# Optimization experiments

Measured on AMD Instinct MI355X. Metric: run time of the kernel, lower is better.

## Reference

```python
import jax, jax.numpy as jnp
import numpy as np

L, B, N, D, H, INTER = 4, 64, 128, 1024, 16, 4096
HD = D // H
EPS = 1e-12


def layer_norm(x, g, b):
    m = jnp.mean(x, axis=-1, keepdims=True)
    v = jnp.mean(jnp.square(x - m), axis=-1, keepdims=True)
    return (x - m) * jax.lax.rsqrt(v + EPS) * g + b


def fast_self_attention(x, wq_w, wq_b, wk_w, wk_b, hwq, hwk, tr_w, tr_b):
    # x: [B, T, D]
    Bq, T, _ = x.shape
    q = x @ wq_w + wq_b                                  # [B,T,D]
    hq = q.reshape(Bq, T, H, HD).transpose(0, 2, 1, 3)    # [B,H,T,hd]
    # additive attention over queries (mask scores are all-zero here)
    alpha = jax.nn.softmax(jnp.einsum('bhtd,hd->bht', hq, hwq) / np.sqrt(HD), axis=-1)
    gq = jnp.einsum('bht,bhtd->bhd', alpha, hq).reshape(Bq, 1, D)  # global query [B,1,D]
    k = x @ wk_w + wk_b
    p = k * gq                                            # [B,T,D]
    hp = p.reshape(Bq, T, H, HD).transpose(0, 2, 1, 3)
    beta = jax.nn.softmax(jnp.einsum('bhtd,hd->bht', hp, hwk) / np.sqrt(HD), axis=-1)
    gk = jnp.einsum('bht,bhtd->bhd', beta, hp).reshape(Bq, 1, D)   # global key [B,1,D]
    u = q * gk
    r = u @ tr_w + tr_b
    return r + q


def encoder_layer(x, p, i):
    a = fast_self_attention(x, p['wq_w'][i], p['wq_b'][i], p['wk_w'][i], p['wk_b'][i],
                            p['hwq'][i], p['hwk'][i], p['tr_w'][i], p['tr_b'][i])
    a = a @ p['so_w'][i] + p['so_b'][i]
    a = layer_norm(a, p['ln1_g'][i], p['ln1_b'][i])
    h = jax.nn.gelu(a @ p['int_w'][i] + p['int_b'][i], approximate=False)
    o = h @ p['out_w'][i] + p['out_b'][i]
    return layer_norm(o + a, p['ln2_g'][i], p['ln2_b'][i])


def setup_inputs() -> dict:
    key = jax.random.key(0)
    ks = iter(jax.random.split(key, 32))
    s = 0.02
    inp = {
        'x': jax.random.normal(next(ks), (B, N, D), jnp.float32),
        'wq_w': jax.random.normal(next(ks), (L, D, D)) * s,
        'wq_b': jnp.zeros((L, D)),
        'wk_w': jax.random.normal(next(ks), (L, D, D)) * s,
        'wk_b': jnp.zeros((L, D)),
        'hwq': jax.random.normal(next(ks), (L, H, HD)) * s,
        'hwk': jax.random.normal(next(ks), (L, H, HD)) * s,
        'tr_w': jax.random.normal(next(ks), (L, D, D)) * s,
        'tr_b': jnp.zeros((L, D)),
        'so_w': jax.random.normal(next(ks), (L, D, D)) * s,
        'so_b': jnp.zeros((L, D)),
        'ln1_g': jnp.ones((L, D)),
        'ln1_b': jnp.zeros((L, D)),
        'int_w': jax.random.normal(next(ks), (L, D, INTER)) * s,
        'int_b': jnp.zeros((L, INTER)),
        'out_w': jax.random.normal(next(ks), (L, INTER, D)) * s,
        'out_b': jnp.zeros((L, D)),
        'ln2_g': jnp.ones((L, D)),
        'ln2_b': jnp.zeros((L, D)),
        'pool_w': jax.random.normal(next(ks), (D, D)) * s,
        'pool_b': jnp.zeros((D,)),
        'pool_q': jax.random.normal(next(ks), (D,)) * s,
    }
    return inp


def reference(x, wq_w, wq_b, wk_w, wk_b, hwq, hwk, tr_w, tr_b, so_w, so_b,
              ln1_g, ln1_b, int_w, int_b, out_w, out_b, ln2_g, ln2_b,
              pool_w, pool_b, pool_q):
    p = dict(wq_w=wq_w, wq_b=wq_b, wk_w=wk_w, wk_b=wk_b, hwq=hwq, hwk=hwk,
             tr_w=tr_w, tr_b=tr_b, so_w=so_w, so_b=so_b, ln1_g=ln1_g, ln1_b=ln1_b,
             int_w=int_w, int_b=int_b, out_w=out_w, out_b=out_b, ln2_g=ln2_g, ln2_b=ln2_b)
    h = x
    for i in range(L):
        h = encoder_layer(h, p, i)
    # additive attention pooling (mask scores are zeros)
    scores = jnp.tanh(h @ pool_w + pool_b) @ pool_q       # [B,N]
    w = jax.nn.softmax(scores, axis=-1)
    return jnp.einsum('bn,bnd->bd', w, h)                 # [B,D]
```

## Files before the change

### kernel.cpp

```cpp
#include <hip/hip_runtime.h>
#include <hip/hip_bf16.h>
#include <math.h>

typedef unsigned short u16;
typedef __attribute__((ext_vector_type(4))) unsigned short u16x4;
typedef __attribute__((ext_vector_type(8))) unsigned short u16x8;
typedef __attribute__((ext_vector_type(8))) short s16x8;
typedef __attribute__((ext_vector_type(4))) float f32x4;

typedef const __attribute__((address_space(1))) void* gas_t;
typedef __attribute__((address_space(3))) void* las_t;

#define DI __device__ __forceinline__

static constexpr int Bc = 64, Nc = 128, Dc = 1024, Hc = 16, HDc = 64, Ic = 4096, Lc = 4;
static constexpr int Mrows = Bc * Nc;

DI float b2f(u16 u) { union { unsigned i; float f; } x; x.i = ((unsigned)u) << 16; return x.f; }
DI u16 f2b(float f) {
  union { float f; unsigned i; } x; x.f = f;
  unsigned r = x.i + 0x7FFF + ((x.i >> 16) & 1);
  return (u16)(r >> 16);
}

#define BARRIER do { asm volatile("" ::: "memory"); __builtin_amdgcn_s_barrier(); asm volatile("" ::: "memory"); } while (0)
#define VMC(N) asm volatile("s_waitcnt vmcnt(" #N ")" ::: "memory")

#define STG(PTR, ROW0, T, SLOT) do { \
    const u16* _s = (PTR) + (size_t)((ROW0) + srow) * K + (((T) << 6) + scol); \
    __builtin_amdgcn_global_load_lds((gas_t)_s, (las_t)(smem + (SLOT) + ldsw), 16, 0, 0); \
    __builtin_amdgcn_global_load_lds((gas_t)(_s + ((size_t)K << 3)), (las_t)(smem + (SLOT) + ldsw + 1024), 16, 0, 0); \
  } while (0)

#define LDA(BUFB, RH) do { \
    _Pragma("unroll") \
    for (int mi = 0; mi < 4; ++mi) { \
      af[mi][0] = *(const s16x8*)(smem + (BUFB) + Abase_rd + (RH) * 8192 + mi * 2048 + aoff0); \
      af[mi][1] = *(const s16x8*)(smem + (BUFB) + Abase_rd + (RH) * 8192 + mi * 2048 + aoff1); \
    } } while (0)

#define LDB(DST, BUFB, CH) do { \
    _Pragma("unroll") \
    for (int nj = 0; nj < 2; ++nj) { \
      DST[nj][0] = *(const s16x8*)(smem + (BUFB) + Bbase_rd + (CH) * 4096 + nj * 2048 + aoff0); \
      DST[nj][1] = *(const s16x8*)(smem + (BUFB) + Bbase_rd + (CH) * 4096 + nj * 2048 + aoff1); \
    } } while (0)

#define MFMAQ(RH, CH, BF) do { \
    __builtin_amdgcn_s_setprio(1); \
    _Pragma("unroll") \
    for (int kk = 0; kk < 2; ++kk) \
      _Pragma("unroll") \
      for (int mi = 0; mi < 4; ++mi) \
        _Pragma("unroll") \
        for (int nj = 0; nj < 2; ++nj) \
          acc[(RH) * 4 + mi][(CH) * 2 + nj] = __builtin_amdgcn_mfma_f32_16x16x32_bf16( \
              af[mi][kk], BF[nj][kk], acc[(RH) * 4 + mi][(CH) * 2 + nj], 0, 0, 0); \
    __builtin_amdgcn_s_setprio(0); \
  } while (0)

template <int EPI, bool SPLIT>
__global__ __launch_bounds__(512, 2) void gemm256(
    const u16* __restrict__ A, const u16* __restrict__ BT,
    const float* __restrict__ bias, const float* __restrict__ bias2,
    const u16* __restrict__ resid, u16* __restrict__ C, u16* __restrict__ C2,
    int M, int N, int K, int NC) {
  extern __shared__ __align__(16) char smem[];
  const int tid = threadIdx.x;
  const int l = tid & 63;
  const int w = tid >> 6;
  const int wr = w >> 2, wc = w & 3;

  const int GX = gridDim.x;
  int wg = blockIdx.y * GX + blockIdx.x;
  const int nwg = GX * gridDim.y;
  wg = (wg & 7) * (nwg >> 3) + (wg >> 3);
  const int bn0 = (wg % GX) * 256;
  const int bm0 = (wg / GX) * 256;

  const int NT = K >> 6;
  const int NI = NT >> 1;

  const int row_l = l & 15;
  const int kl = (l >> 4) * 8;
  const int xr = (row_l & 7) << 3;
  const int aoff0 = row_l * 128 + (((0 * 32 + kl) ^ xr) * 2);
  const int aoff1 = row_l * 128 + (((1 * 32 + kl) ^ xr) * 2);
  const int Abase_rd = wr * 16384;
  const int Bbase_rd = 32768 + (wc >> 1) * 16384 + (wc & 1) * 8192;

  const int srow = w * 16 + (l >> 3);
  const int scol = ((l & 7) ^ ((l >> 3) & 7)) << 3;
  const int ldsw = w * 2048;

  enum { b0A0 = 0, b0A1 = 16384, b0B0 = 32768, b0B1 = 49152,
         b1A0 = 65536, b1A1 = 81920, b1B0 = 98304, b1B1 = 114688 };

  STG(BT, bn0, 0, b0B0);
  STG(BT, bn0 + 128, 0, b0B1);
  STG(A, bm0, 0, b0A0);
  STG(A, bm0 + 128, 0, b0A1);
  STG(BT, bn0, 1, b1B0);
  STG(BT, bn0 + 128, 1, b1B1);
  VMC(4);
  BARRIER;

  f32x4 acc[8][4];
#pragma unroll
  for (int i = 0; i < 8; ++i)
#pragma unroll
    for (int j = 0; j < 4; ++j) acc[i][j] = f32x4{0.f, 0.f, 0.f, 0.f};
  s16x8 af[4][2], bf0[2][2], bf1[2][2];

  for (int j = 0; j < NI; ++j) {
    const int t1 = 2 * j + 1;
    int t2 = 2 * j + 2; if (t2 >= NT) t2 = 0;
    int t3 = 2 * j + 3; if (t3 >= NT) t3 = 1;
    LDA(0, 0); LDB(bf0, 0, 0);
    STG(A, bm0, t1, b1A0);
    BARRIER; MFMAQ(0, 0, bf0); BARRIER;
    LDB(bf1, 0, 1);
    STG(A, bm0 + 128, t1, b1A1);
    BARRIER; MFMAQ(0, 1, bf1); BARRIER;
    LDA(0, 1);
    STG(BT, bn0, t2, b0B0);
    BARRIER; MFMAQ(1, 0, bf0); BARRIER;
    STG(BT, bn0 + 128, t2, b0B1);
    STG(A, bm0, t2, b0A0);
    VMC(6);
    BARRIER; MFMAQ(1, 1, bf1); BARRIER;
    LDA(65536, 0); LDB(bf0, 65536, 0);
    STG(A, bm0 + 128, t2, b0A1);
    BARRIER; MFMAQ(0, 0, bf0); BARRIER;
    LDB(bf1, 65536, 1);
    BARRIER; MFMAQ(0, 1, bf1); BARRIER;
    LDA(65536, 1);
    STG(BT, bn0, t3, b1B0);
    BARRIER; MFMAQ(1, 0, bf0); BARRIER;
    STG(BT, bn0 + 128, t3, b1B1);
    VMC(4);
    BARRIER; MFMAQ(1, 1, bf1); BARRIER;
  }

  u16* Cout = C;
  const float* bi = bias;
  int cb = bn0;
  if (SPLIT) {
    const int half = N >> 1;
    if (bn0 >= half) { Cout = C2; bi = bias2; cb = bn0 - half; }
  }
  const int r0 = bm0 + wr * 128 + ((l >> 4) << 2);
#pragma unroll
  for (int fi = 0; fi < 8; ++fi) {
#pragma unroll
    for (int fj = 0; fj < 4; ++fj) {
      const int ocol = cb + wc * 64 + fj * 16 + (l & 15);
      const float bv = bi[ocol];
      const int row = r0 + fi * 16;
#pragma unroll
      for (int r = 0; r < 4; ++r) {
        float v = acc[fi][fj][r] + bv;
        if constexpr (EPI == 1) v += b2f(resid[(size_t)(row + r) * NC + ocol]);
        if constexpr (EPI == 2) v = 0.5f * v * (1.f + erff(v * 0.70710678118654752f));
        if constexpr (EPI == 3) v = tanhf(v);
        Cout[(size_t)(row + r) * NC + ocol] = f2b(v);
      }
    }
  }
}

#define LDA2(BUFB, RH) do { \
    _Pragma("unroll") \
    for (int mi = 0; mi < 2; ++mi) { \
      af[mi][0] = *(const s16x8*)(smem + (BUFB) + Abase_rd + ((RH) * 2 + mi) * 2048 + aoff0); \
      af[mi][1] = *(const s16x8*)(smem + (BUFB) + Abase_rd + ((RH) * 2 + mi) * 2048 + aoff1); \
    } } while (0)

#define MFMAQ2(RH, CH, BF) do { \
    __builtin_amdgcn_s_setprio(1); \
    _Pragma("unroll") \
    for (int kk = 0; kk < 2; ++kk) \
      _Pragma("unroll") \
      for (int mi = 0; mi < 2; ++mi) \
        _Pragma("unroll") \
        for (int nj = 0; nj < 2; ++nj) \
          acc[(RH) * 2 + mi][(CH) * 2 + nj] = __builtin_amdgcn_mfma_f32_16x16x32_bf16( \
              af[mi][kk], BF[nj][kk], acc[(RH) * 2 + mi][(CH) * 2 + nj], 0, 0, 0); \
    __builtin_amdgcn_s_setprio(0); \
  } while (0)

template <int EPI>
__global__ __launch_bounds__(512, 2) void gemm128n(
    const u16* __restrict__ A, const u16* __restrict__ BT,
    const float* __restrict__ bias, const u16* __restrict__ resid,
    u16* __restrict__ C, int M, int N, int K, int NC) {
  extern __shared__ __align__(16) char smem[];
  const int tid = threadIdx.x;
  const int l = tid & 63;
  const int w = tid >> 6;
  const int wr = w >> 1, wc = w & 1;

  const int GX = gridDim.x;
  int wg = blockIdx.y * GX + blockIdx.x;
  const int nwg = GX * gridDim.y;
  wg = (wg & 7) * (nwg >> 3) + (wg >> 3);
  const int bn0 = (wg % GX) * 128;
  const int bm0 = (wg / GX) * 256;

  const int NT = K >> 6;
  const int NI = NT >> 1;

  const int row_l = l & 15;
  const int kl = (l >> 4) * 8;
  const int xr = (row_l & 7) << 3;
  const int aoff0 = row_l * 128 + (((0 * 32 + kl) ^ xr) * 2);
  const int aoff1 = row_l * 128 + (((1 * 32 + kl) ^ xr) * 2);
  const int Abase_rd = (wr >> 1) * 16384 + (wr & 1) * 8192;
  const int Bbase_rd = 32768 + wc * 8192;

  const int srow = w * 16 + (l >> 3);
  const int scol = ((l & 7) ^ ((l >> 3) & 7)) << 3;
  const int ldsw = w * 2048;

  enum { c0A0 = 0, c0A1 = 16384, c0B = 32768,
         c1A0 = 49152, c1A1 = 65536, c1B = 81920 };

  STG(BT, bn0, 0, c0B);
  STG(A, bm0, 0, c0A0);
  STG(A, bm0 + 128, 0, c0A1);
  STG(BT, bn0, 1, c1B);
  VMC(2);
  BARRIER;

  f32x4 acc[4][4];
#pragma unroll
  for (int i = 0; i < 4; ++i)
#pragma unroll
    for (int j = 0; j < 4; ++j) acc[i][j] = f32x4{0.f, 0.f, 0.f, 0.f};
  s16x8 af[2][2], bf0[2][2], bf1[2][2];

  for (int j = 0; j < NI; ++j) {
    const int t1 = 2 * j + 1;
    int t2 = 2 * j + 2; if (t2 >= NT) t2 = 0;
    int t3 = 2 * j + 3; if (t3 >= NT) t3 = 1;
    LDA2(0, 0); LDB(bf0, 0, 0);
    STG(A, bm0, t1, c1A0);
    BARRIER; MFMAQ2(0, 0, bf0); BARRIER;
    LDB(bf1, 0, 1);
    STG(A, bm0 + 128, t1, c1A1);
    BARRIER; MFMAQ2(0, 1, bf1); BARRIER;
    LDA2(0, 1);
    STG(BT, bn0, t2, c0B);
    BARRIER; MFMAQ2(1, 0, bf0); BARRIER;
    STG(A, bm0, t2, c0A0);
    VMC(4);
    BARRIER; MFMAQ2(1, 1, bf1); BARRIER;
    LDA2(49152, 0); LDB(bf0, 49152, 0);
    STG(A, bm0 + 128, t2, c0A1);
    BARRIER; MFMAQ2(0, 0, bf0); BARRIER;
    LDB(bf1, 49152, 1);
    BARRIER; MFMAQ2(0, 1, bf1); BARRIER;
    LDA2(49152, 1);
    STG(BT, bn0, t3, c1B);
    BARRIER; MFMAQ2(1, 0, bf0); BARRIER;
    VMC(2);
    BARRIER; MFMAQ2(1, 1, bf1); BARRIER;
  }

  const int r0 = bm0 + wr * 64 + ((l >> 4) << 2);
#pragma unroll
  for (int fi = 0; fi < 4; ++fi) {
#pragma unroll
    for (int fj = 0; fj < 4; ++fj) {
      const int ocol = bn0 + wc * 64 + fj * 16 + (l & 15);
      const float bv = bias[ocol];
      const int row = r0 + fi * 16;
#pragma unroll
      for (int r = 0; r < 4; ++r) {
        float v = acc[fi][fj][r] + bv;
        if constexpr (EPI == 1) v += b2f(resid[(size_t)(row + r) * NC + ocol]);
        if constexpr (EPI == 2) v = 0.5f * v * (1.f + erff(v * 0.70710678118654752f));
        if constexpr (EPI == 3) v = tanhf(v);
        C[(size_t)(row + r) * NC + ocol] = f2b(v);
      }
    }
  }
}

DI void ttile(const float* in, u16* out, int R, int C, int r0, int c0, int t) {
  __shared__ u16 tile[32][33];
  const int lr = t >> 3;
  const int lc = (t & 7) * 4;
  f32x4 v = *(const f32x4*)(in + (size_t)(r0 + lr) * C + c0 + lc);
#pragma unroll
  for (int j = 0; j < 4; ++j) tile[lr][lc + j] = f2b(v[j]);
  __syncthreads();
  u16x4 o;
#pragma unroll
  for (int j = 0; j < 4; ++j) o[j] = tile[lc + j][lr];
  *(u16x4*)(out + (size_t)(c0 + lr) * R + r0 + lc) = o;
}

__global__ __launch_bounds__(256) void transpose_cvt(
    const float* __restrict__ in, u16* __restrict__ out, int R, int C) {
  ttile(in, out, R, C, blockIdx.y * 32, blockIdx.x * 32, threadIdx.x);
}

__global__ __launch_bounds__(256) void transpose4sq(
    const float* s0, const float* s1, const float* s2, const float* s3,
    u16* d0, u16* d1, u16* d2, u16* d3) {
  const int z = blockIdx.z;
  const float* in = z == 0 ? s0 : z == 1 ? s1 : z == 2 ? s2 : s3;
  u16* out = z == 0 ? d0 : z == 1 ? d1 : z == 2 ? d2 : d3;
  ttile(in, out, 1024, 1024, blockIdx.y * 32, blockIdx.x * 32, threadIdx.x);
}

__global__ __launch_bounds__(256) void transpose_io(
    const float* si, u16* di, const float* so, u16* dout) {
  if (blockIdx.z == 0) {
    ttile(si, di, 1024, 4096, blockIdx.y * 32, blockIdx.x * 32, threadIdx.x);
  } else {
    ttile(so, dout, 4096, 1024, blockIdx.x * 32, blockIdx.y * 32, threadIdx.x);
  }
}

__global__ __launch_bounds__(256) void cvt_k(
    const float* __restrict__ in, u16* __restrict__ out) {
  const size_t i = ((size_t)blockIdx.x * 256 + threadIdx.x) * 8;
  f32x4 a = *(const f32x4*)(in + i);
  f32x4 b = *(const f32x4*)(in + i + 4);
  u16x8 o;
#pragma unroll
  for (int j = 0; j < 4; ++j) o[j] = f2b(a[j]);
#pragma unroll
  for (int j = 0; j < 4; ++j) o[4 + j] = f2b(b[j]);
  *(u16x8*)(out + i) = o;
}

__global__ __launch_bounds__(128) void attn_fused(
    const u16* __restrict__ q, const u16* __restrict__ k,
    const float* __restrict__ hwq, const float* __restrict__ hwk,
    u16* __restrict__ u) {
  const int bh = blockIdx.x;
  const int b = bh >> 4, h = bh & 15;
  const int tid = threadIdx.x;
  const int lane = tid & 63, wv = tid >> 6;
  const int d = tid & 63, half = tid >> 6;
  __shared__ u16 qt[128][68];
  __shared__ u16 kt[128][68];
  __shared__ float hw[64];
  __shared__ float gqs[64];
  __shared__ float gks[64];
  __shared__ float ex[128];
  __shared__ float part[64];
  __shared__ float xw[4];

  const int rw8 = tid >> 3;
  const int cg8 = (tid & 7) * 8;
#pragma unroll
  for (int pass = 0; pass < 8; ++pass) {
    const int row = pass * 16 + rw8;
    const size_t off = (size_t)(b * 128 + row) * Dc + h * 64 + cg8;
    u16x8 vq = *(const u16x8*)(q + off);
    u16x8 vk = *(const u16x8*)(k + off);
    u16x4 q0{vq[0], vq[1], vq[2], vq[3]}, q1{vq[4], vq[5], vq[6], vq[7]};
    u16x4 k0{vk[0], vk[1], vk[2], vk[3]}, k1{vk[4], vk[5], vk[6], vk[7]};
    *(u16x4*)&qt[row][cg8] = q0;
    *(u16x4*)&qt[row][cg8 + 4] = q1;
    *(u16x4*)&kt[row][cg8] = k0;
    *(u16x4*)&kt[row][cg8 + 4] = k1;
  }
  if (tid < 64) hw[tid] = hwq[h * 64 + tid];
  __syncthreads();

  float s = 0.f;
#pragma unroll
  for (int c = 0; c < 16; ++c) {
    u16x4 v = *(const u16x4*)&qt[tid][c * 4];
#pragma unroll
    for (int j = 0; j < 4; ++j) s += b2f(v[j]) * hw[c * 4 + j];
  }
  s *= 0.125f;
  float m = s;
  for (int o = 32; o; o >>= 1) m = fmaxf(m, __shfl_xor(m, o));
  if (lane == 0) xw[wv] = m;
  __syncthreads();
  m = fmaxf(xw[0], xw[1]);
  float e = __expf(s - m);
  ex[tid] = e;
  float sm = e;
  for (int o = 32; o; o >>= 1) sm += __shfl_xor(sm, o);
  if (lane == 0) xw[2 + wv] = sm;
  __syncthreads();
  float sum = xw[2] + xw[3];
  {
    float acc = 0.f;
    for (int t = 0; t < 64; ++t) acc += ex[half * 64 + t] * b2f(qt[half * 64 + t][d]);
    if (half == 0) part[d] = acc;
    __syncthreads();
    if (half == 1) gqs[d] = (part[d] + acc) / sum;
  }
  __syncthreads();

  if (tid < 64) hw[tid] = hwk[h * 64 + tid];
  __syncthreads();
  s = 0.f;
#pragma unroll
  for (int c = 0; c < 16; ++c) {
    u16x4 v = *(const u16x4*)&kt[tid][c * 4];
#pragma unroll
    for (int j = 0; j < 4; ++j) s += b2f(v[j]) * gqs[c * 4 + j] * hw[c * 4 + j];
  }
  s *= 0.125f;
  m = s;
  for (int o = 32; o; o >>= 1) m = fmaxf(m, __shfl_xor(m, o));
  if (lane == 0) xw[wv] = m;
  __syncthreads();
  m = fmaxf(xw[0], xw[1]);
  e = __expf(s - m);
  ex[tid] = e;
  sm = e;
  for (int o = 32; o; o >>= 1) sm += __shfl_xor(sm, o);
  if (lane == 0) xw[2 + wv] = sm;
  __syncthreads();
  sum = xw[2] + xw[3];
  {
    float acc = 0.f;
    for (int t = 0; t < 64; ++t) acc += ex[half * 64 + t] * b2f(kt[half * 64 + t][d]);
    acc *= gqs[d];
    if (half == 0) part[d] = acc;
    __syncthreads();
    if (half == 1) gks[d] = (part[d] + acc) / sum;
  }
  __syncthreads();

#pragma unroll
  for (int pass = 0; pass < 8; ++pass) {
    const int row = pass * 16 + rw8;
    u16x4 a = *(const u16x4*)&qt[row][cg8];
    u16x4 bb = *(const u16x4*)&qt[row][cg8 + 4];
    u16x8 o;
#pragma unroll
    for (int j = 0; j < 4; ++j) o[j] = f2b(b2f(a[j]) * gks[cg8 + j]);
#pragma unroll
    for (int j = 0; j < 4; ++j) o[4 + j] = f2b(b2f(bb[j]) * gks[cg8 + 4 + j]);
    *(u16x8*)(u + (size_t)(b * 128 + row) * Dc + h * 64 + cg8) = o;
  }
}

__global__ __launch_bounds__(256) void ln_k(
    const u16* __restrict__ in, const float* __restrict__ g,
    const float* __restrict__ bta, u16* __restrict__ out) {
  const int row = blockIdx.x, tid = threadIdx.x;
  const int lane = tid & 63, wave = tid >> 6;
  __shared__ float red[8];
  const u16* p = in + (size_t)row * Dc + tid * 4;
  u16x4 v = *(const u16x4*)p;
  float x[4];
  float s = 0.f, sq = 0.f;
#pragma unroll
  for (int j = 0; j < 4; ++j) {
    x[j] = b2f(v[j]);
    s += x[j];
    sq += x[j] * x[j];
  }
  for (int o = 32; o; o >>= 1) {
    s += __shfl_down(s, o);
    sq += __shfl_down(sq, o);
  }
  if (lane == 0) {
    red[wave] = s;
    red[4 + wave] = sq;
  }
  __syncthreads();
  s = red[0] + red[1] + red[2] + red[3];
  sq = red[4] + red[5] + red[6] + red[7];
  const float mean = s * (1.f / 1024.f);
  const float var = sq * (1.f / 1024.f) - mean * mean;
  const float rs = rsqrtf(var + 1e-12f);
  f32x4 gv = *(const f32x4*)(g + tid * 4);
  f32x4 bv = *(const f32x4*)(bta + tid * 4);
  u16x4 o;
#pragma unroll
  for (int j = 0; j < 4; ++j) o[j] = f2b((x[j] - mean) * rs * gv[j] + bv[j]);
  *(u16x4*)(out + (size_t)row * Dc + tid * 4) = o;
}

__global__ __launch_bounds__(256) void pool_k(
    const u16* __restrict__ s1, const float* __restrict__ pq,
    const u16* __restrict__ h, float* __restrict__ out) {
  const int b = blockIdx.x, tid = threadIdx.x;
  __shared__ float pqs[1024];
  __shared__ float sc[128];
  __shared__ float ex[128];
  for (int i = tid; i < 1024; i += 256) pqs[i] = pq[i];
  __syncthreads();
  if (tid < 128) {
    const u16* row = s1 + ((size_t)(b * 128 + tid)) * Dc;
    float s = 0.f;
    for (int c = 0; c < 128; ++c) {
      u16x8 v = *(const u16x8*)(row + c * 8);
#pragma unroll
      for (int j = 0; j < 8; ++j) s += b2f(v[j]) * pqs[c * 8 + j];
    }
    sc[tid] = s;
  }
  __syncthreads();
  float m = -1e30f;
  for (int t = 0; t < 128; ++t) m = fmaxf(m, sc[t]);
  if (tid < 128) ex[tid] = __expf(sc[tid] - m);
  __syncthreads();
  float sum = 0.f;
  for (int t = 0; t < 128; ++t) sum += ex[t];
  const int d0 = tid * 4;
  float acc[4] = {0.f, 0.f, 0.f, 0.f};
  for (int n = 0; n < 128; ++n) {
    const float w = ex[n];
    u16x4 v = *(const u16x4*)(h + ((size_t)(b * 128 + n)) * Dc + d0);
#pragma unroll
    for (int j = 0; j < 4; ++j) acc[j] += w * b2f(v[j]);
  }
  const float inv = 1.f / sum;
  f32x4 o;
#pragma unroll
  for (int j = 0; j < 4; ++j) o[j] = acc[j] * inv;
  *(f32x4*)(out + b * Dc + d0) = o;
}

extern "C" void kernel_launch(void* const* d_in, const int* in_sizes, int n_in,
                              void* d_out, int out_size, void* d_ws, size_t ws_size,
                              hipStream_t stream) {
  const float* x = (const float*)d_in[0];
  const float* wq_w = (const float*)d_in[1];
  const float* wq_b = (const float*)d_in[2];
  const float* wk_w = (const float*)d_in[3];
  const float* wk_b = (const float*)d_in[4];
  const float* hwq = (const float*)d_in[5];
  const float* hwk = (const float*)d_in[6];
  const float* tr_w = (const float*)d_in[7];
  const float* tr_b = (const float*)d_in[8];
  const float* so_w = (const float*)d_in[9];
  const float* so_b = (const float*)d_in[10];
  const float* ln1g = (const float*)d_in[11];
  const float* ln1b = (const float*)d_in[12];
  const float* int_w = (const float*)d_in[13];
  const float* int_b = (const float*)d_in[14];
  const float* out_w = (const float*)d_in[15];
  const float* out_b = (const float*)d_in[16];
  const float* ln2g = (const float*)d_in[17];
  const float* ln2b = (const float*)d_in[18];
  const float* pool_w = (const float*)d_in[19];
  const float* pool_b = (const float*)d_in[20];
  const float* pool_q = (const float*)d_in[21];

  char* w = (char*)d_ws;
  auto alloc = [&](size_t bytes) {
    char* p = w;
    w += (bytes + 255) & ~(size_t)255;
    return p;
  };
  u16* wTqk = (u16*)alloc((size_t)2 * Dc * Dc * 2);
  u16* wTtr = (u16*)alloc((size_t)Dc * Dc * 2);
  u16* wTso = (u16*)alloc((size_t)Dc * Dc * 2);
  u16* wTint = (u16*)alloc((size_t)Dc * Ic * 2);
  u16* wTout = (u16*)alloc((size_t)Dc * Ic * 2);
  u16* wTpool = (u16*)alloc((size_t)Dc * Dc * 2);
  u16* qb = (u16*)alloc((size_t)Mrows * Dc * 2);
  u16* kb = (u16*)alloc((size_t)Mrows * Dc * 2);
  u16* ab = (u16*)alloc((size_t)Mrows * Dc * 2);
  u16* tb = (u16*)alloc((size_t)Mrows * Dc * 2);
  u16* xc = (u16*)alloc((size_t)Mrows * Dc * 2);
  u16* hb = (u16*)alloc((size_t)Mrows * Ic * 2);
  if ((size_t)(w - (char*)d_ws) > ws_size) return;

  static constexpr size_t LDSB = 131072;
  static constexpr size_t LDSB2 = 98304;
  hipFuncSetAttribute((const void*)gemm256<0, true>, hipFuncAttributeMaxDynamicSharedMemorySize, LDSB);
  hipFuncSetAttribute((const void*)gemm256<2, false>, hipFuncAttributeMaxDynamicSharedMemorySize, LDSB);
  hipFuncSetAttribute((const void*)gemm128n<0>, hipFuncAttributeMaxDynamicSharedMemorySize, LDSB2);
  hipFuncSetAttribute((const void*)gemm128n<1>, hipFuncAttributeMaxDynamicSharedMemorySize, LDSB2);
  hipFuncSetAttribute((const void*)gemm128n<3>, hipFuncAttributeMaxDynamicSharedMemorySize, LDSB2);

  const dim3 blk(256);
  const dim3 blkG(512);
  const dim3 gT1(Dc / 32, Dc / 32);
  const dim3 gT4(Dc / 32, Dc / 32, 4);
  const dim3 gTio(Ic / 32, Dc / 32, 2);
  const dim3 gQK(2048 / 256, Mrows / 256);
  const dim3 gNi(Ic / 256, Mrows / 256);
  const dim3 gO(Dc / 128, Mrows / 256);

  cvt_k<<<(Mrows * Dc) / (256 * 8), blk, 0, stream>>>(x, xc);

  for (int i = 0; i < Lc; ++i) {
    transpose4sq<<<gT4, blk, 0, stream>>>(
        wq_w + (size_t)i * Dc * Dc, wk_w + (size_t)i * Dc * Dc,
        tr_w + (size_t)i * Dc * Dc, so_w + (size_t)i * Dc * Dc,
        wTqk, wTqk + (size_t)Dc * Dc, wTtr, wTso);
    transpose_io<<<gTio, blk, 0, stream>>>(
        int_w + (size_t)i * Dc * Ic, wTint, out_w + (size_t)i * Ic * Dc, wTout);

    gemm256<0, true><<<gQK, blkG, LDSB, stream>>>(xc, wTqk, wq_b + i * Dc, wk_b + i * Dc,
                                                  nullptr, qb, kb, Mrows, 2048, Dc, Dc);
    attn_fused<<<Bc * Hc, 128, 0, stream>>>(qb, kb, hwq + i * Hc * HDc,
                                            hwk + i * Hc * HDc, kb);
    gemm128n<1><<<gO, blkG, LDSB2, stream>>>(kb, wTtr, tr_b + i * Dc, qb, tb, Mrows, Dc, Dc, Dc);
    gemm128n<0><<<gO, blkG, LDSB2, stream>>>(tb, wTso, so_b + i * Dc, nullptr, kb, Mrows, Dc, Dc, Dc);
    ln_k<<<Mrows, blk, 0, stream>>>(kb, ln1g + i * Dc, ln1b + i * Dc, ab);
    gemm256<2, false><<<gNi, blkG, LDSB, stream>>>(ab, wTint, int_b + i * Ic, nullptr,
                                                   nullptr, hb, nullptr, Mrows, Ic, Dc, Ic);
    gemm128n<1><<<gO, blkG, LDSB2, stream>>>(hb, wTout, out_b + i * Dc, ab, tb, Mrows, Dc, Ic, Dc);
    ln_k<<<Mrows, blk, 0, stream>>>(tb, ln2g + i * Dc, ln2b + i * Dc, xc);
  }

  transpose_cvt<<<gT1, blk, 0, stream>>>(pool_w, wTpool, Dc, Dc);
  gemm128n<3><<<gO, blkG, LDSB2, stream>>>(xc, wTpool, pool_b, nullptr, tb, Mrows, Dc, Dc, Dc);
  pool_k<<<Bc, blk, 0, stream>>>(tb, pool_q, xc, (float*)d_out);
}
```

Before: 1.209 ms.

## Use 4-wave 256x256 GEMM with 128x128 per-wave tiles for QK and intermediate

Replaces the 8-wave (512-thread) 256x256 GEMM with a 4-wave (256-thread) variant in which each wave computes a 128x128 sub-tile (8x8 MFMA accumulators). Each thread now issues four direct-to-LDS loads per stage instead of two, and the vmcnt waits are adjusted to match. The goal is more MFMA work per LDS fragment load and fewer waves contending at barriers. The cost is far higher register pressure (256 accumulator floats per thread), one workgroup per CU, and less latency hiding.

After: 1.632 ms. 35.0% more time.

```diff
diff --git a/kernel.cpp b/kernel.cpp
--- a/kernel.cpp
+++ b/kernel.cpp
@@ -32,35 +32,43 @@
     __builtin_amdgcn_global_load_lds((gas_t)(_s + ((size_t)K << 3)), (las_t)(smem + (SLOT) + ldsw + 1024), 16, 0, 0); \
   } while (0)
 
-#define LDA(BUFB, RH) do { \
+#define STG4(PTR, ROW0, T, SLOT) do { \
+    const u16* _s = (PTR) + (size_t)((ROW0) + srow) * K + (((T) << 6) + scol); \
+    __builtin_amdgcn_global_load_lds((gas_t)_s, (las_t)(smem + (SLOT) + ldsw), 16, 0, 0); \
+    __builtin_amdgcn_global_load_lds((gas_t)(_s + ((size_t)K << 3)), (las_t)(smem + (SLOT) + ldsw + 1024), 16, 0, 0); \
+    __builtin_amdgcn_global_load_lds((gas_t)(_s + ((size_t)K << 4)), (las_t)(smem + (SLOT) + ldsw + 2048), 16, 0, 0); \
+    __builtin_amdgcn_global_load_lds((gas_t)(_s + 24 * (size_t)K), (las_t)(smem + (SLOT) + ldsw + 3072), 16, 0, 0); \
+  } while (0)
+
+#define LDAW(BUFB, RH) do { \
     _Pragma("unroll") \
     for (int mi = 0; mi < 4; ++mi) { \
       af[mi][0] = *(const s16x8*)(smem + (BUFB) + Abase_rd + (RH) * 8192 + mi * 2048 + aoff0); \
       af[mi][1] = *(const s16x8*)(smem + (BUFB) + Abase_rd + (RH) * 8192 + mi * 2048 + aoff1); \
     } } while (0)
 
-#define LDB(DST, BUFB, CH) do { \
+#define LDBW(DST, BUFB, CH) do { \
     _Pragma("unroll") \
-    for (int nj = 0; nj < 2; ++nj) { \
-      DST[nj][0] = *(const s16x8*)(smem + (BUFB) + Bbase_rd + (CH) * 4096 + nj * 2048 + aoff0); \
-      DST[nj][1] = *(const s16x8*)(smem + (BUFB) + Bbase_rd + (CH) * 4096 + nj * 2048 + aoff1); \
+    for (int nj = 0; nj < 4; ++nj) { \
+      DST[nj][0] = *(const s16x8*)(smem + (BUFB) + Bbase_rd + (CH) * 8192 + nj * 2048 + aoff0); \
+      DST[nj][1] = *(const s16x8*)(smem + (BUFB) + Bbase_rd + (CH) * 8192 + nj * 2048 + aoff1); \
     } } while (0)
 
-#define MFMAQ(RH, CH, BF) do { \
+#define MFMAW(RH, CH, BF) do { \
     __builtin_amdgcn_s_setprio(1); \
     _Pragma("unroll") \
     for (int kk = 0; kk < 2; ++kk) \
       _Pragma("unroll") \
       for (int mi = 0; mi < 4; ++mi) \
         _Pragma("unroll") \
-        for (int nj = 0; nj < 2; ++nj) \
-          acc[(RH) * 4 + mi][(CH) * 2 + nj] = __builtin_amdgcn_mfma_f32_16x16x32_bf16( \
-              af[mi][kk], BF[nj][kk], acc[(RH) * 4 + mi][(CH) * 2 + nj], 0, 0, 0); \
+        for (int nj = 0; nj < 4; ++nj) \
+          acc[(RH) * 4 + mi][(CH) * 4 + nj] = __builtin_amdgcn_mfma_f32_16x16x32_bf16( \
+              af[mi][kk], BF[nj][kk], acc[(RH) * 4 + mi][(CH) * 4 + nj], 0, 0, 0); \
     __builtin_amdgcn_s_setprio(0); \
   } while (0)
 
 template <int EPI, bool SPLIT>
-__global__ __launch_bounds__(512, 2) void gemm256(
+__global__ __launch_bounds__(256, 1) void gemm256w(
     const u16* __restrict__ A, const u16* __restrict__ BT,
     const float* __restrict__ bias, const float* __restrict__ bias2,
     const u16* __restrict__ resid, u16* __restrict__ C, u16* __restrict__ C2,
@@ -69,7 +77,7 @@
   const int tid = threadIdx.x;
   const int l = tid & 63;
   const int w = tid >> 6;
-  const int wr = w >> 2, wc = w & 3;
+  const int wr = w >> 1, wc = w & 1;
 
   const int GX = gridDim.x;
   int wg = blockIdx.y * GX + blockIdx.x;
@@ -87,59 +95,59 @@
   const int aoff0 = row_l * 128 + (((0 * 32 + kl) ^ xr) * 2);
   const int aoff1 = row_l * 128 + (((1 * 32 + kl) ^ xr) * 2);
   const int Abase_rd = wr * 16384;
-  const int Bbase_rd = 32768 + (wc >> 1) * 16384 + (wc & 1) * 8192;
-
-  const int srow = w * 16 + (l >> 3);
+  const int Bbase_rd = 32768 + wc * 16384;
+
+  const int srow = w * 32 + (l >> 3);
   const int scol = ((l & 7) ^ ((l >> 3) & 7)) << 3;
-  const int ldsw = w * 2048;
+  const int ldsw = w * 4096;
 
   enum { b0A0 = 0, b0A1 = 16384, b0B0 = 32768, b0B1 = 49152,
          b1A0 = 65536, b1A1 = 81920, b1B0 = 98304, b1B1 = 114688 };
 
-  STG(BT, bn0, 0, b0B0);
-  STG(BT, bn0 + 128, 0, b0B1);
-  STG(A, bm0, 0, b0A0);
-  STG(A, bm0 + 128, 0, b0A1);
-  STG(BT, bn0, 1, b1B0);
-  STG(BT, bn0 + 128, 1, b1B1);
-  VMC(4);
+  STG4(BT, bn0, 0, b0B0);
+  STG4(BT, bn0 + 128, 0, b0B1);
+  STG4(A, bm0, 0, b0A0);
+  STG4(A, bm0 + 128, 0, b0A1);
+  STG4(BT, bn0, 1, b1B0);
+  STG4(BT, bn0 + 128, 1, b1B1);
+  VMC(8);
   BARRIER;
 
-  f32x4 acc[8][4];
+  f32x4 acc[8][8];
 #pragma unroll
   for (int i = 0; i < 8; ++i)
 #pragma unroll
-    for (int j = 0; j < 4; ++j) acc[i][j] = f32x4{0.f, 0.f, 0.f, 0.f};
-  s16x8 af[4][2], bf0[2][2], bf1[2][2];
+    for (int j = 0; j < 8; ++j) acc[i][j] = f32x4{0.f, 0.f, 0.f, 0.f};
+  s16x8 af[4][2], bf0[4][2], bf1[4][2];
 
   for (int j = 0; j < NI; ++j) {
     const int t1 = 2 * j + 1;
     int t2 = 2 * j + 2; if (t2 >= NT) t2 = 0;
     int t3 = 2 * j + 3; if (t3 >= NT) t3 = 1;
-    LDA(0, 0); LDB(bf0, 0, 0);
-    STG(A, bm0, t1, b1A0);
-    BARRIER; MFMAQ(0, 0, bf0); BARRIER;
-    LDB(bf1, 0, 1);
-    STG(A, bm0 + 128, t1, b1A1);
-    BARRIER; MFMAQ(0, 1, bf1); BARRIER;
-    LDA(0, 1);
-    STG(BT, bn0, t2, b0B0);
-    BARRIER; MFMAQ(1, 0, bf0); BARRIER;
-    STG(BT, bn0 + 128, t2, b0B1);
-    STG(A, bm0, t2, b0A0);
-    VMC(6);
-    BARRIER; MFMAQ(1, 1, bf1); BARRIER;
-    LDA(65536, 0); LDB(bf0, 65536, 0);
-    STG(A, bm0 + 128, t2, b0A1);
-    BARRIER; MFMAQ(0, 0, bf0); BARRIER;
-    LDB(bf1, 65536, 1);
-    BARRIER; MFMAQ(0, 1, bf1); BARRIER;
-    LDA(65536, 1);
-    STG(BT, bn0, t3, b1B0);
-    BARRIER; MFMAQ(1, 0, bf0); BARRIER;
-    STG(BT, bn0 + 128, t3, b1B1);
-    VMC(4);
-    BARRIER; MFMAQ(1, 1, bf1); BARRIER;
+    LDAW(0, 0); LDBW(bf0, 0, 0);
+    STG4(A, bm0, t1, b1A0);
+    BARRIER; MFMAW(0, 0, bf0); BARRIER;
+    LDBW(bf1, 0, 1);
+    STG4(A, bm0 + 128, t1, b1A1);
+    BARRIER; MFMAW(0, 1, bf1); BARRIER;
+    LDAW(0, 1);
+    STG4(BT, bn0, t2, b0B0);
+    BARRIER; MFMAW(1, 0, bf0); BARRIER;
+    STG4(BT, bn0 + 128, t2, b0B1);
+    STG4(A, bm0, t2, b0A0);
+    VMC(12);
+    BARRIER; MFMAW(1, 1, bf1); BARRIER;
+    LDAW(65536, 0); LDBW(bf0, 65536, 0);
+    STG4(A, bm0 + 128, t2, b0A1);
+    BARRIER; MFMAW(0, 0, bf0); BARRIER;
+    LDBW(bf1, 65536, 1);
+    BARRIER; MFMAW(0, 1, bf1); BARRIER;
+    LDAW(65536, 1);
+    STG4(BT, bn0, t3, b1B0);
+    BARRIER; MFMAW(1, 0, bf0); BARRIER;
+    STG4(BT, bn0 + 128, t3, b1B1);
+    VMC(8);
+    BARRIER; MFMAW(1, 1, bf1); BARRIER;
   }
 
   u16* Cout = C;
@@ -153,8 +161,8 @@
 #pragma unroll
   for (int fi = 0; fi < 8; ++fi) {
 #pragma unroll
-    for (int fj = 0; fj < 4; ++fj) {
-      const int ocol = cb + wc * 64 + fj * 16 + (l & 15);
+    for (int fj = 0; fj < 8; ++fj) {
+      const int ocol = cb + wc * 128 + fj * 16 + (l & 15);
       const float bv = bi[ocol];
       const int row = r0 + fi * 16;
 #pragma unroll
@@ -168,6 +176,13 @@
     }
   }
 }
+
+#define LDB(DST, BUFB, CH) do { \
+    _Pragma("unroll") \
+    for (int nj = 0; nj < 2; ++nj) { \
+      DST[nj][0] = *(const s16x8*)(smem + (BUFB) + Bbase_rd + (CH) * 4096 + nj * 2048 + aoff0); \
+      DST[nj][1] = *(const s16x8*)(smem + (BUFB) + Bbase_rd + (CH) * 4096 + nj * 2048 + aoff1); \
+    } } while (0)
 
 #define LDA2(BUFB, RH) do { \
     _Pragma("unroll") \
@@ -575,14 +590,15 @@
 
   static constexpr size_t LDSB = 131072;
   static constexpr size_t LDSB2 = 98304;
-  hipFuncSetAttribute((const void*)gemm256<0, true>, hipFuncAttributeMaxDynamicSharedMemorySize, LDSB);
-  hipFuncSetAttribute((const void*)gemm256<2, false>, hipFuncAttributeMaxDynamicSharedMemorySize, LDSB);
+  hipFuncSetAttribute((const void*)gemm256w<0, true>, hipFuncAttributeMaxDynamicSharedMemorySize, LDSB);
+  hipFuncSetAttribute((const void*)gemm256w<2, false>, hipFuncAttributeMaxDynamicSharedMemorySize, LDSB);
   hipFuncSetAttribute((const void*)gemm128n<0>, hipFuncAttributeMaxDynamicSharedMemorySize, LDSB2);
   hipFuncSetAttribute((const void*)gemm128n<1>, hipFuncAttributeMaxDynamicSharedMemorySize, LDSB2);
   hipFuncSetAttribute((const void*)gemm128n<3>, hipFuncAttributeMaxDynamicSharedMemorySize, LDSB2);
 
   const dim3 blk(256);
   const dim3 blkG(512);
+  const dim3 blkW(256);
   const dim3 gT1(Dc / 32, Dc / 32);
   const dim3 gT4(Dc / 32, Dc / 32, 4);
   const dim3 gTio(Ic / 32, Dc / 32, 2);
@@ -600,15 +616,15 @@
     transpose_io<<<gTio, blk, 0, stream>>>(
         int_w + (size_t)i * Dc * Ic, wTint, out_w + (size_t)i * Ic * Dc, wTout);
 
-    gemm256<0, true><<<gQK, blkG, LDSB, stream>>>(xc, wTqk, wq_b + i * Dc, wk_b + i * Dc,
-                                                  nullptr, qb, kb, Mrows, 2048, Dc, Dc);
+    gemm256w<0, true><<<gQK, blkW, LDSB, stream>>>(xc, wTqk, wq_b + i * Dc, wk_b + i * Dc,
+                                                   nullptr, qb, kb, Mrows, 2048, Dc, Dc);
     attn_fused<<<Bc * Hc, 128, 0, stream>>>(qb, kb, hwq + i * Hc * HDc,
                                             hwk + i * Hc * HDc, kb);
     gemm128n<1><<<gO, blkG, LDSB2, stream>>>(kb, wTtr, tr_b + i * Dc, qb, tb, Mrows, Dc, Dc, Dc);
     gemm128n<0><<<gO, blkG, LDSB2, stream>>>(tb, wTso, so_b + i * Dc, nullptr, kb, Mrows, Dc, Dc, Dc);
     ln_k<<<Mrows, blk, 0, stream>>>(kb, ln1g + i * Dc, ln1b + i * Dc, ab);
-    gemm256<2, false><<<gNi, blkG, LDSB, stream>>>(ab, wTint, int_b + i * Ic, nullptr,
-                                                   nullptr, hb, nullptr, Mrows, Ic, Dc, Ic);
+    gemm256w<2, false><<<gNi, blkW, LDSB, stream>>>(ab, wTint, int_b + i * Ic, nullptr,
+                                                    nullptr, hb, nullptr, Mrows, Ic, Dc, Ic);
     gemm128n<1><<<gO, blkG, LDSB2, stream>>>(hb, wTout, out_b + i * Dc, ab, tb, Mrows, Dc, Ic, Dc);
     ln_k<<<Mrows, blk, 0, stream>>>(tb, ln2g + i * Dc, ln2b + i * Dc, xc);
   }
```
